# Kernel optimization log

Measured on AMD Instinct MI355X. Metric: run time of the kernel, lower is better.

## Reference

```python
import jax, jax.numpy as jnp
import numpy as np

N = 50000
NEG_SLOPE = 0.2
BN_EPS = 1e-5


def _self_loops(src, dst, n):
    loop = jnp.arange(n, dtype=src.dtype)
    return jnp.concatenate([src, loop]), jnp.concatenate([dst, loop])


def gcn_conv(x, src, dst, W, b, n):
    # PyG GCNConv: add self-loops, symmetric deg^-1/2 normalization, scatter-add.
    h = x @ W                                             # [N, C]
    s, d = _self_loops(src, dst, n)
    deg = jax.ops.segment_sum(jnp.ones_like(d, dtype=h.dtype), d, num_segments=n)
    dinv = jnp.where(deg > 0, jax.lax.rsqrt(deg), 0.0)
    norm = dinv[s] * dinv[d]                              # [E+N]
    out = jax.ops.segment_sum(h[s] * norm[:, None], d, num_segments=n)
    return out + b


def gat_conv(x, src, dst, W, a_src, a_dst, b, n, heads):
    # PyG GATConv (concat=False, eval mode: no dropout): add self-loops,
    # per-edge LeakyReLU attention logits, segment-softmax over dst, mean heads.
    C = W.shape[1] // heads
    h = (x @ W).reshape(n, heads, C)                      # [N, H, C]
    s, d = _self_loops(src, dst, n)
    al_s = jnp.sum(h * a_src[None], axis=-1)              # [N, H]
    al_d = jnp.sum(h * a_dst[None], axis=-1)              # [N, H]
    e = jax.nn.leaky_relu(al_s[s] + al_d[d], NEG_SLOPE)   # [E+N, H]
    emax = jax.ops.segment_max(e, d, num_segments=n)[d]
    ex = jnp.exp(e - emax)
    denom = jax.ops.segment_sum(ex, d, num_segments=n)[d]
    alpha = ex / denom                                    # [E+N, H]
    out = jax.ops.segment_sum(h[s] * alpha[:, :, None], d, num_segments=n)
    return jnp.mean(out, axis=1) + b                      # concat=False -> head mean


def batch_norm(x, g, b, m, v):
    # eval-mode BatchNorm1d with running stats
    return (x - m) * jax.lax.rsqrt(v + BN_EPS) * g + b


def setup_inputs() -> dict:
    key = jax.random.key(0)
    ks = jax.random.split(key, 12)
    E = 800000
    inp = {}
    inp['x'] = jax.random.normal(ks[0], (N, 128), dtype=jnp.float32)
    inp['edge_index'] = jax.random.randint(ks[1], (2, E), 0, N, dtype=jnp.int64)
    inp['gcn1_W'] = jax.random.normal(ks[2], (128, 96), dtype=jnp.float32) * 0.08
    inp['gcn1_b'] = jnp.zeros((96,), jnp.float32)
    inp['bn1_g'] = jnp.ones((96,), jnp.float32)
    inp['bn1_b'] = jnp.zeros((96,), jnp.float32)
    inp['bn1_m'] = jnp.zeros((96,), jnp.float32)
    inp['bn1_v'] = jnp.ones((96,), jnp.float32)
    inp['gat1_W'] = jax.random.normal(ks[3], (96, 192), dtype=jnp.float32) * 0.1
    inp['gat1_as'] = jax.random.normal(ks[4], (2, 96), dtype=jnp.float32) * 0.1
    inp['gat1_ad'] = jax.random.normal(ks[5], (2, 96), dtype=jnp.float32) * 0.1
    inp['gat1_b'] = jnp.zeros((96,), jnp.float32)
    inp['gcn2_W'] = jax.random.normal(ks[6], (96, 96), dtype=jnp.float32) * 0.1
    inp['gcn2_b'] = jnp.zeros((96,), jnp.float32)
    inp['bn2_g'] = jnp.ones((96,), jnp.float32)
    inp['bn2_b'] = jnp.zeros((96,), jnp.float32)
    inp['bn2_m'] = jnp.zeros((96,), jnp.float32)
    inp['bn2_v'] = jnp.ones((96,), jnp.float32)
    inp['gat2_W'] = jax.random.normal(ks[7], (96, 80), dtype=jnp.float32) * 0.1
    inp['gat2_as'] = jax.random.normal(ks[8], (2, 40), dtype=jnp.float32) * 0.1
    inp['gat2_ad'] = jax.random.normal(ks[9], (2, 40), dtype=jnp.float32) * 0.1
    inp['gat2_b'] = jnp.zeros((40,), jnp.float32)
    return inp


def reference(x, edge_index, gcn1_W, gcn1_b, bn1_g, bn1_b, bn1_m, bn1_v,
              gat1_W, gat1_as, gat1_ad, gat1_b, gcn2_W, gcn2_b,
              bn2_g, bn2_b, bn2_m, bn2_v, gat2_W, gat2_as, gat2_ad, gat2_b):
    src, dst = edge_index[0], edge_index[1]
    h = gcn_conv(x, src, dst, gcn1_W, gcn1_b, N)
    h = jax.nn.relu(batch_norm(h, bn1_g, bn1_b, bn1_m, bn1_v))
    h = jax.nn.relu(gat_conv(h, src, dst, gat1_W, gat1_as, gat1_ad, gat1_b, N, 2))
    h = gcn_conv(h, src, dst, gcn2_W, gcn2_b, N)
    h = jax.nn.relu(batch_norm(h, bn2_g, bn2_b, bn2_m, bn2_v))
    h = gat_conv(h, src, dst, gat2_W, gat2_as, gat2_ad, gat2_b, N, 2)
    return jax.nn.log_softmax(h, axis=1)
```

## Files before the change

### kernel.cpp

```cpp
#include <hip/hip_runtime.h>
#include <math.h>

#define NNODES 50000
#define NEG_SLOPE 0.2f
#define BN_EPS 1e-5f

typedef __attribute__((ext_vector_type(8))) short bf16x8;
typedef __attribute__((ext_vector_type(4))) float f32x4;

static __device__ __forceinline__ float leaky(float x) {
    return x > 0.f ? x : NEG_SLOPE * x;
}
static __device__ __forceinline__ unsigned short f2bf(float x) {
    unsigned u = __float_as_uint(x);
    u += 0x7FFFu + ((u >> 16) & 1u);
    return (unsigned short)(u >> 16);
}
static __device__ __forceinline__ void unpack8(uint4 u, float* v) {
    v[0] = __uint_as_float(u.x << 16);
    v[1] = __uint_as_float(u.x & 0xFFFF0000u);
    v[2] = __uint_as_float(u.y << 16);
    v[3] = __uint_as_float(u.y & 0xFFFF0000u);
    v[4] = __uint_as_float(u.z << 16);
    v[5] = __uint_as_float(u.z & 0xFFFF0000u);
    v[6] = __uint_as_float(u.w << 16);
    v[7] = __uint_as_float(u.w & 0xFFFF0000u);
}
static __device__ __forceinline__ void acc8(uint4 u, float w, float* a) {
    float v[8]; unpack8(u, v);
#pragma unroll
    for (int j = 0; j < 8; ++j) a[j] = fmaf(w, v[j], a[j]);
}
static __device__ __forceinline__ uint4 pack8(const float* o) {
    uint4 r;
    r.x = ((unsigned)f2bf(o[1]) << 16) | f2bf(o[0]);
    r.y = ((unsigned)f2bf(o[3]) << 16) | f2bf(o[2]);
    r.z = ((unsigned)f2bf(o[5]) << 16) | f2bf(o[4]);
    r.w = ((unsigned)f2bf(o[7]) << 16) | f2bf(o[6]);
    return r;
}

__global__ void k_count(const int* __restrict__ dst, int* degi, int E) {
    int e = blockIdx.x * blockDim.x + threadIdx.x;
    if (e < E) atomicAdd(&degi[dst[e]], 1);
}
__global__ void k_scan1(const int* __restrict__ degi, int* __restrict__ incl,
                        int* __restrict__ bsum, int n) {
    __shared__ int s[256];
    int i = blockIdx.x * 256 + threadIdx.x;
    int v = (i < n) ? degi[i] : 0;
    s[threadIdx.x] = v;
    __syncthreads();
    for (int off = 1; off < 256; off <<= 1) {
        int t = (threadIdx.x >= (unsigned)off) ? s[threadIdx.x - off] : 0;
        __syncthreads();
        s[threadIdx.x] += t;
        __syncthreads();
    }
    if (i < n) incl[i] = s[threadIdx.x];
    if (threadIdx.x == 255) bsum[blockIdx.x] = s[255];
}
__global__ void k_scan2(int* bsum, int nb) {
    __shared__ int s[256];
    int v = ((int)threadIdx.x < nb) ? bsum[threadIdx.x] : 0;
    s[threadIdx.x] = v;
    __syncthreads();
    for (int off = 1; off < 256; off <<= 1) {
        int t = (threadIdx.x >= (unsigned)off) ? s[threadIdx.x - off] : 0;
        __syncthreads();
        s[threadIdx.x] += t;
        __syncthreads();
    }
    if ((int)threadIdx.x < nb) bsum[threadIdx.x] = s[threadIdx.x];
}
__global__ void k_scan3(const int* __restrict__ degi, const int* __restrict__ incl,
                        const int* __restrict__ bsum, int* __restrict__ row_ptr,
                        int* __restrict__ cursor, float* __restrict__ dinv, int n) {
    int i = blockIdx.x * 256 + threadIdx.x;
    if (i >= n) return;
    int off = (blockIdx.x > 0) ? bsum[blockIdx.x - 1] : 0;
    int inc = incl[i] + off;
    row_ptr[i + 1] = inc;
    cursor[i] = inc - degi[i];
    dinv[i] = rsqrtf((float)(degi[i] + 1));
    if (i == 0) row_ptr[0] = 0;
}
__global__ void k_fill(const int* __restrict__ src, const int* __restrict__ dst,
                       int* cursor, int* __restrict__ csr_src, int E) {
    int e = blockIdx.x * blockDim.x + threadIdx.x;
    if (e >= E) return;
    int pos = atomicAdd(&cursor[dst[e]], 1);
    csr_src[pos] = src[e];
}

__global__ void k_wconv(const float* __restrict__ W, unsigned short* __restrict__ out,
                        int Ki, int Ko) {
    int idx = blockIdx.x * blockDim.x + threadIdx.x;
    if (idx >= Ki * Ko) return;
    int k = idx / Ko, c = idx % Ko;
    out[c * Ki + k] = f2bf(W[idx]);
}
__global__ void k_xconv(const float4* __restrict__ x, uint4* __restrict__ out, int n8) {
    int i = blockIdx.x * blockDim.x + threadIdx.x;
    if (i >= n8) return;
    float4 a = x[i * 2], b = x[i * 2 + 1];
    float o[8] = {a.x, a.y, a.z, a.w, b.x, b.y, b.z, b.w};
    out[i] = pack8(o);
}

template<int KI, int KO>
__launch_bounds__(256)
__global__ void k_gemm_mfma(const unsigned short* __restrict__ A,
                            const unsigned short* __restrict__ WT,
                            unsigned short* __restrict__ C, int n) {
    constexpr int KP = KI + 8;
    constexpr int NT = KO / 16;
    constexpr int KT = KI / 32;
    __shared__ unsigned short wT[KO][KP];
    const int t = threadIdx.x;
    const int w = t >> 6, l = t & 63;

    constexpr int CH = KI / 8;
    for (int idx = t; idx < KO * CH; idx += 256) {
        int r = idx / CH, o = idx % CH;
        *(uint4*)&wT[r][o * 8] = *(const uint4*)&WT[r * KI + o * 8];
    }
    int row = blockIdx.x * 64 + w * 16 + (l & 15);
    bool rv = row < n;
    const unsigned short* ap = A + (long long)row * KI + (l >> 4) * 8;
    bf16x8 afr[KT];
#pragma unroll
    for (int kt = 0; kt < KT; ++kt) {
        bf16x8 z = {};
        afr[kt] = rv ? *(const bf16x8*)(ap + kt * 32) : z;
    }
    __syncthreads();

    f32x4 acc[NT];
#pragma unroll
    for (int ct = 0; ct < NT; ++ct) acc[ct] = (f32x4){0.f, 0.f, 0.f, 0.f};
#pragma unroll
    for (int kt = 0; kt < KT; ++kt) {
#pragma unroll
        for (int ct = 0; ct < NT; ++ct) {
            bf16x8 b = *(const bf16x8*)&wT[ct * 16 + (l & 15)][kt * 32 + (l >> 4) * 8];
            acc[ct] = __builtin_amdgcn_mfma_f32_16x16x32_bf16(afr[kt], b, acc[ct], 0, 0, 0);
        }
    }
    int orow0 = blockIdx.x * 64 + w * 16 + (l >> 4) * 4;
    int col = l & 15;
#pragma unroll
    for (int ct = 0; ct < NT; ++ct) {
#pragma unroll
        for (int r = 0; r < 4; ++r) {
            int rr = orow0 + r;
            if (rr < n) C[(long long)rr * KO + ct * 16 + col] = f2bf(acc[ct][r]);
        }
    }
}

__global__ void k_gcn_gather_bn8(const uint4* __restrict__ hb, const int* __restrict__ row_ptr,
                                 const int* __restrict__ csr_src, const float* __restrict__ dinv,
                                 const float* __restrict__ bias, const float* __restrict__ g,
                                 const float* __restrict__ b, const float* __restrict__ m,
                                 const float* __restrict__ vv,
                                 uint4* __restrict__ outb, int n, int Q8) {
    int t = blockIdx.x * blockDim.x + threadIdx.x;
    if (t >= n * Q8) return;
    int v = t / Q8, q = t % Q8;
    int beg = row_ptr[v], end = row_ptr[v + 1];
    float dv = dinv[v];
    float a[8] = {0.f, 0.f, 0.f, 0.f, 0.f, 0.f, 0.f, 0.f};
    acc8(hb[(long long)v * Q8 + q], dv, a);
    int p = beg;
    for (; p + 4 <= end; p += 4) {
        int s0 = csr_src[p], s1 = csr_src[p + 1], s2 = csr_src[p + 2], s3 = csr_src[p + 3];
        float w0 = dinv[s0], w1 = dinv[s1], w2 = dinv[s2], w3 = dinv[s3];
        uint4 u0 = hb[(long long)s0 * Q8 + q];
        uint4 u1 = hb[(long long)s1 * Q8 + q];
        uint4 u2 = hb[(long long)s2 * Q8 + q];
        uint4 u3 = hb[(long long)s3 * Q8 + q];
        acc8(u0, w0, a);
        acc8(u1, w1, a);
        acc8(u2, w2, a);
        acc8(u3, w3, a);
    }
    for (; p < end; ++p) {
        int s = csr_src[p];
        acc8(hb[(long long)s * Q8 + q], dinv[s], a);
    }
    int c0 = q * 8;
    float o[8];
#pragma unroll
    for (int j = 0; j < 8; ++j) {
        int c = c0 + j;
        float x = fmaf(a[j], dv, bias[c]);
        x = (x - m[c]) * rsqrtf(vv[c] + BN_EPS) * g[c] + b[c];
        o[j] = fmaxf(x, 0.f);
    }
    outb[(long long)v * Q8 + q] = pack8(o);
}

__global__ void k_gat_logits8(const uint4* __restrict__ hb, const float* __restrict__ as,
                              const float* __restrict__ ad, float* __restrict__ alS,
                              float* __restrict__ alD, int n, int C) {
    int t = blockIdx.x * blockDim.x + threadIdx.x;
    if (t >= n * 2) return;
    int hh = t & 1;
    int C8 = C >> 3;
    const uint4* row = hb + (long long)t * C8;
    float s1 = 0.f, s2 = 0.f;
    for (int q = 0; q < C8; ++q) {
        float v[8]; unpack8(row[q], v);
#pragma unroll
        for (int j = 0; j < 8; ++j) {
            int c = hh * C + q * 8 + j;
            s1 = fmaf(v[j], as[c], s1);
            s2 = fmaf(v[j], ad[c], s2);
        }
    }
    alS[t] = s1; alD[t] = s2;
}
__global__ void k_gat_vh2p(const int* __restrict__ row_ptr, const int* __restrict__ csr_src,
                           const float2* __restrict__ alS2, const float2* __restrict__ alD2,
                           float2* __restrict__ eex2, float2* __restrict__ selfw2,
                           float2* __restrict__ invden2, int n) {
    int v = blockIdx.x * blockDim.x + threadIdx.x;
    if (v >= n) return;
    int beg = row_ptr[v], end = row_ptr[v + 1];
    float2 ad = alD2[v], as0 = alS2[v];
    float ls0 = leaky(as0.x + ad.x), ls1 = leaky(as0.y + ad.y);
    float m0 = ls0, m1 = ls1;
    int p = beg;
    for (; p + 2 <= end; p += 2) {
        int s0 = csr_src[p], s1 = csr_src[p + 1];
        float2 a0 = alS2[s0], a1 = alS2[s1];
        float l00 = leaky(a0.x + ad.x), l01 = leaky(a0.y + ad.y);
        float l10 = leaky(a1.x + ad.x), l11 = leaky(a1.y + ad.y);
        eex2[p] = make_float2(l00, l01);
        eex2[p + 1] = make_float2(l10, l11);
        m0 = fmaxf(m0, fmaxf(l00, l10));
        m1 = fmaxf(m1, fmaxf(l01, l11));
    }
    if (p < end) {
        int s = csr_src[p];
        float2 a = alS2[s];
        float l0 = leaky(a.x + ad.x), l1 = leaky(a.y + ad.y);
        eex2[p] = make_float2(l0, l1);
        m0 = fmaxf(m0, l0);
        m1 = fmaxf(m1, l1);
    }
    float e0 = expf(ls0 - m0), e1 = expf(ls1 - m1);
    float d0 = e0, d1 = e1;
    for (p = beg; p < end; ++p) {
        float2 l = eex2[p];
        float x0 = expf(l.x - m0), x1 = expf(l.y - m1);
        eex2[p] = make_float2(x0, x1);
        d0 += x0; d1 += x1;
    }
    selfw2[v] = make_float2(e0, e1);
    invden2[v] = make_float2(1.f / d0, 1.f / d1);
}
template<int OUTBF>
__global__ void k_gat_gather2_8(const uint4* __restrict__ hb, const int* __restrict__ row_ptr,
                                const int* __restrict__ csr_src, const float2* __restrict__ eex2,
                                const float2* __restrict__ selfw2, const float2* __restrict__ invden2,
                                const float* __restrict__ bias, uint4* __restrict__ outb,
                                float4* __restrict__ outf, int n, int Q8, int do_relu) {
    int t = blockIdx.x * blockDim.x + threadIdx.x;
    if (t >= n * Q8) return;
    int v = t / Q8, q = t % Q8;
    int rowOct = 2 * Q8;
    int beg = row_ptr[v], end = row_ptr[v + 1];
    float A0[8] = {0,0,0,0,0,0,0,0}, A1[8] = {0,0,0,0,0,0,0,0};
    {
        float2 sw = selfw2[v];
        const uint4* hv = hb + (long long)v * rowOct;
        acc8(hv[q], sw.x, A0);
        acc8(hv[Q8 + q], sw.y, A1);
    }
    int p = beg;
    for (; p + 4 <= end; p += 4) {
        int s0 = csr_src[p], s1 = csr_src[p + 1], s2 = csr_src[p + 2], s3 = csr_src[p + 3];
        float2 w0 = eex2[p], w1 = eex2[p + 1], w2 = eex2[p + 2], w3 = eex2[p + 3];
        const uint4* h0 = hb + (long long)s0 * rowOct;
        const uint4* h1 = hb + (long long)s1 * rowOct;
        const uint4* h2 = hb + (long long)s2 * rowOct;
        const uint4* h3 = hb + (long long)s3 * rowOct;
        uint4 u00 = h0[q], u01 = h0[Q8 + q];
        uint4 u10 = h1[q], u11 = h1[Q8 + q];
        uint4 u20 = h2[q], u21 = h2[Q8 + q];
        uint4 u30 = h3[q], u31 = h3[Q8 + q];
        acc8(u00, w0.x, A0); acc8(u01, w0.y, A1);
        acc8(u10, w1.x, A0); acc8(u11, w1.y, A1);
        acc8(u20, w2.x, A0); acc8(u21, w2.y, A1);
        acc8(u30, w3.x, A0); acc8(u31, w3.y, A1);
    }
    for (; p < end; ++p) {
        int s = csr_src[p];
        float2 w = eex2[p];
        const uint4* hs = hb + (long long)s * rowOct;
        acc8(hs[q], w.x, A0);
        acc8(hs[Q8 + q], w.y, A1);
    }
    float2 idn = invden2[v];
    int c0 = q * 8;
    float o[8];
#pragma unroll
    for (int j = 0; j < 8; ++j) {
        float x = fmaf(0.5f, fmaf(A0[j], idn.x, A1[j] * idn.y), bias[c0 + j]);
        o[j] = do_relu ? fmaxf(x, 0.f) : x;
    }
    if (OUTBF) {
        outb[(long long)v * Q8 + q] = pack8(o);
    } else {
        long long ob = (long long)v * (Q8 * 2) + q * 2;
        outf[ob]     = make_float4(o[0], o[1], o[2], o[3]);
        outf[ob + 1] = make_float4(o[4], o[5], o[6], o[7]);
    }
}

__global__ void k_logsoftmax40(const float* __restrict__ in, float* __restrict__ out, int n) {
    int v = blockIdx.x * blockDim.x + threadIdx.x;
    if (v >= n) return;
    float vals[40];
    float mx = -INFINITY;
#pragma unroll
    for (int c = 0; c < 40; ++c) {
        float x = in[v * 40 + c];
        vals[c] = x;
        mx = fmaxf(mx, x);
    }
    float s = 0.f;
#pragma unroll
    for (int c = 0; c < 40; ++c) s += expf(vals[c] - mx);
    float ls = logf(s);
#pragma unroll
    for (int c = 0; c < 40; ++c) out[v * 40 + c] = vals[c] - mx - ls;
}

static inline int nblk(long long n, int b) { return (int)((n + b - 1) / b); }

extern "C" void kernel_launch(void* const* d_in, const int* in_sizes, int n_in,
                              void* d_out, int out_size, void* d_ws, size_t ws_size,
                              hipStream_t stream) {
    const float* x       = (const float*)d_in[0];
    const int*   ei      = (const int*)d_in[1];
    const float* gcn1_W  = (const float*)d_in[2];
    const float* gcn1_b  = (const float*)d_in[3];
    const float* bn1_g   = (const float*)d_in[4];
    const float* bn1_b   = (const float*)d_in[5];
    const float* bn1_m   = (const float*)d_in[6];
    const float* bn1_v   = (const float*)d_in[7];
    const float* gat1_W  = (const float*)d_in[8];
    const float* gat1_as = (const float*)d_in[9];
    const float* gat1_ad = (const float*)d_in[10];
    const float* gat1_b  = (const float*)d_in[11];
    const float* gcn2_W  = (const float*)d_in[12];
    const float* gcn2_b  = (const float*)d_in[13];
    const float* bn2_g   = (const float*)d_in[14];
    const float* bn2_b   = (const float*)d_in[15];
    const float* bn2_m   = (const float*)d_in[16];
    const float* bn2_v   = (const float*)d_in[17];
    const float* gat2_W  = (const float*)d_in[18];
    const float* gat2_as = (const float*)d_in[19];
    const float* gat2_ad = (const float*)d_in[20];
    const float* gat2_b  = (const float*)d_in[21];

    const int n = NNODES;
    const int E = in_sizes[1] / 2;
    const int* src = ei;
    const int* dst = ei + E;

    char* p = (char*)d_ws;
    float* dinv    = (float*)p; p += 50048 * 4;
    int*   degi    = (int*)p;   p += 50048 * 4;
    int*   row_ptr = (int*)p;   p += 50052 * 4;
    int*   cursor  = (int*)p;   p += 50048 * 4;
    int*   incl    = (int*)p;   p += 50048 * 4;
    int*   bsum    = (int*)p;   p += 256 * 4;
    int*   csr_src = (int*)p;   p += 800000 * 4;
    unsigned short* hbf = (unsigned short*)p; p += 9600000 * 2;
    unsigned short* abf = (unsigned short*)p; p += 6400000 * 2;
    unsigned short* wbf = (unsigned short*)p; p += 47616 * 2 + 64;
    float* bufA    = (float*)p; p += 2000000 * 4;
    float* alS     = (float*)p; p += 100096 * 4;
    float* alD     = (float*)p; p += 100096 * 4;
    float* selfw   = (float*)p; p += 100096 * 4;
    float* invden  = (float*)p; p += 100096 * 4;
    float* eex     = (float*)p; p += 1600000 * 4;

    unsigned short* w1T = wbf;
    unsigned short* w2T = wbf + 12288;
    unsigned short* w3T = wbf + 12288 + 18432;
    unsigned short* w4T = wbf + 12288 + 18432 + 9216;

    const int B = 256;
    const int GB = nblk(n, 64);
    const int SB = nblk(n, 256);
    float* out = (float*)d_out;

    k_wconv<<<nblk(128 * 96, B), B, 0, stream>>>(gcn1_W, w1T, 128, 96);
    k_wconv<<<nblk(96 * 192, B), B, 0, stream>>>(gat1_W, w2T, 96, 192);
    k_wconv<<<nblk(96 * 96, B), B, 0, stream>>>(gcn2_W, w3T, 96, 96);
    k_wconv<<<nblk(96 * 80, B), B, 0, stream>>>(gat2_W, w4T, 96, 80);
    k_xconv<<<nblk((long long)n * 16, B), B, 0, stream>>>((const float4*)x, (uint4*)abf, n * 16);

    hipMemsetAsync(degi, 0, (size_t)n * 4, stream);
    k_count<<<nblk(E, B), B, 0, stream>>>(dst, degi, E);
    k_scan1<<<SB, 256, 0, stream>>>(degi, incl, bsum, n);
    k_scan2<<<1, 256, 0, stream>>>(bsum, SB);
    k_scan3<<<SB, 256, 0, stream>>>(degi, incl, bsum, row_ptr, cursor, dinv, n);
    k_fill<<<nblk(E, B), B, 0, stream>>>(src, dst, cursor, csr_src, E);

    k_gemm_mfma<128, 96><<<GB, 256, 0, stream>>>(abf, w1T, hbf, n);
    k_gcn_gather_bn8<<<nblk((long long)n * 12, B), B, 0, stream>>>(
        (const uint4*)hbf, row_ptr, csr_src, dinv, gcn1_b, bn1_g, bn1_b, bn1_m, bn1_v,
        (uint4*)abf, n, 12);

    k_gemm_mfma<96, 192><<<GB, 256, 0, stream>>>(abf, w2T, hbf, n);
    k_gat_logits8<<<nblk(n * 2, B), B, 0, stream>>>((const uint4*)hbf, gat1_as, gat1_ad, alS, alD, n, 96);
    k_gat_vh2p<<<nblk(n, B), B, 0, stream>>>(row_ptr, csr_src, (const float2*)alS, (const float2*)alD,
                                             (float2*)eex, (float2*)selfw, (float2*)invden, n);
    k_gat_gather2_8<1><<<nblk((long long)n * 12, B), B, 0, stream>>>(
        (const uint4*)hbf, row_ptr, csr_src, (const float2*)eex, (const float2*)selfw,
        (const float2*)invden, gat1_b, (uint4*)abf, nullptr, n, 12, 1);

    k_gemm_mfma<96, 96><<<GB, 256, 0, stream>>>(abf, w3T, hbf, n);
    k_gcn_gather_bn8<<<nblk((long long)n * 12, B), B, 0, stream>>>(
        (const uint4*)hbf, row_ptr, csr_src, dinv, gcn2_b, bn2_g, bn2_b, bn2_m, bn2_v,
        (uint4*)abf, n, 12);

    k_gemm_mfma<96, 80><<<GB, 256, 0, stream>>>(abf, w4T, hbf, n);
    k_gat_logits8<<<nblk(n * 2, B), B, 0, stream>>>((const uint4*)hbf, gat2_as, gat2_ad, alS, alD, n, 40);
    k_gat_vh2p<<<nblk(n, B), B, 0, stream>>>(row_ptr, csr_src, (const float2*)alS, (const float2*)alD,
                                             (float2*)eex, (float2*)selfw, (float2*)invden, n);
    k_gat_gather2_8<0><<<nblk((long long)n * 5, B), B, 0, stream>>>(
        (const uint4*)hbf, row_ptr, csr_src, (const float2*)eex, (const float2*)selfw,
        (const float2*)invden, gat2_b, nullptr, (float4*)bufA, n, 5, 0);

    k_logsoftmax40<<<nblk(n, B), B, 0, stream>>>(bufA, out, n);
}
```

Baseline: 375.4 us.

## Fuse GAT logits into GEMM epilogue, merge conversions, use nontemporal loads/stores

Computes GAT attention logits inside the MFMA GEMM epilogue from fp32 accumulators using cross-lane shuffles, removing the separate logits kernel and its reread of the bf16 features. Merges the four weight conversions and the x conversion into one launch. Switches streaming CSR/edge-weight loads and output stores to nontemporal hints to reduce cache pollution. Logits now come from fp32 rather than bf16-rounded values, which changes numerics slightly; nontemporal stores of outputs reread by the next GEMM may lose cache reuse.

```diff
diff --git a/kernel.cpp b/kernel.cpp
--- a/kernel.cpp
+++ b/kernel.cpp
@@ -7,6 +7,7 @@
 
 typedef __attribute__((ext_vector_type(8))) short bf16x8;
 typedef __attribute__((ext_vector_type(4))) float f32x4;
+typedef __attribute__((ext_vector_type(4))) unsigned int u32x4;
 
 static __device__ __forceinline__ float leaky(float x) {
     return x > 0.f ? x : NEG_SLOPE * x;
@@ -38,6 +39,19 @@
     r.z = ((unsigned)f2bf(o[5]) << 16) | f2bf(o[4]);
     r.w = ((unsigned)f2bf(o[7]) << 16) | f2bf(o[6]);
     return r;
+}
+static __device__ __forceinline__ int ldnt_i(const int* p) {
+    return __builtin_nontemporal_load(p);
+}
+static __device__ __forceinline__ float2 ldnt_f2(const float2* p) {
+    unsigned long long d = __builtin_nontemporal_load((const unsigned long long*)p);
+    return make_float2(__uint_as_float((unsigned)d), __uint_as_float((unsigned)(d >> 32)));
+}
+static __device__ __forceinline__ void stnt_u4(uint4* p, uint4 v) {
+    __builtin_nontemporal_store(*(u32x4*)&v, (u32x4*)p);
+}
+static __device__ __forceinline__ void stnt_f4(float4* p, float4 v) {
+    __builtin_nontemporal_store(*(f32x4*)&v, (f32x4*)p);
 }
 
 __global__ void k_count(const int* __restrict__ dst, int* degi, int E) {
@@ -93,26 +107,42 @@
     csr_src[pos] = src[e];
 }
 
-__global__ void k_wconv(const float* __restrict__ W, unsigned short* __restrict__ out,
-                        int Ki, int Ko) {
-    int idx = blockIdx.x * blockDim.x + threadIdx.x;
-    if (idx >= Ki * Ko) return;
-    int k = idx / Ko, c = idx % Ko;
-    out[c * Ki + k] = f2bf(W[idx]);
-}
-__global__ void k_xconv(const float4* __restrict__ x, uint4* __restrict__ out, int n8) {
+__global__ void k_convall(const float4* __restrict__ x, uint4* __restrict__ xout,
+                          const float* __restrict__ W1, unsigned short* __restrict__ w1T,
+                          const float* __restrict__ W2, unsigned short* __restrict__ w2T,
+                          const float* __restrict__ W3, unsigned short* __restrict__ w3T,
+                          const float* __restrict__ W4, unsigned short* __restrict__ w4T,
+                          int nx) {
     int i = blockIdx.x * blockDim.x + threadIdx.x;
-    if (i >= n8) return;
-    float4 a = x[i * 2], b = x[i * 2 + 1];
-    float o[8] = {a.x, a.y, a.z, a.w, b.x, b.y, b.z, b.w};
-    out[i] = pack8(o);
-}
-
-template<int KI, int KO>
+    if (i < nx) {
+        float4 a = x[i * 2], b = x[i * 2 + 1];
+        float o[8] = {a.x, a.y, a.z, a.w, b.x, b.y, b.z, b.w};
+        xout[i] = pack8(o);
+        return;
+    }
+    int j = i - nx;
+    if (j < 12288) {
+        int k = j / 96, c = j % 96;
+        w1T[c * 128 + k] = f2bf(W1[j]);
+    } else if ((j -= 12288) < 18432) {
+        int k = j / 192, c = j % 192;
+        w2T[c * 96 + k] = f2bf(W2[j]);
+    } else if ((j -= 18432) < 9216) {
+        int k = j / 96, c = j % 96;
+        w3T[c * 96 + k] = f2bf(W3[j]);
+    } else if ((j -= 9216) < 7680) {
+        int k = j / 80, c = j % 80;
+        w4T[c * 96 + k] = f2bf(W4[j]);
+    }
+}
+
+template<int KI, int KO, int HC>
 __launch_bounds__(256)
 __global__ void k_gemm_mfma(const unsigned short* __restrict__ A,
                             const unsigned short* __restrict__ WT,
-                            unsigned short* __restrict__ C, int n) {
+                            unsigned short* __restrict__ C, int n,
+                            const float* __restrict__ as, const float* __restrict__ ad,
+                            float* __restrict__ alS, float* __restrict__ alD) {
     constexpr int KP = KI + 8;
     constexpr int NT = KO / 16;
     constexpr int KT = KI / 32;
@@ -155,6 +185,38 @@
         for (int r = 0; r < 4; ++r) {
             int rr = orow0 + r;
             if (rr < n) C[(long long)rr * KO + ct * 16 + col] = f2bf(acc[ct][r]);
+        }
+    }
+    if (HC > 0) {
+        float asv[NT], adv[NT];
+#pragma unroll
+        for (int ct = 0; ct < NT; ++ct) {
+            int cg = ct * 16 + col;
+            asv[ct] = as[cg];
+            adv[ct] = ad[cg];
+        }
+#pragma unroll
+        for (int r = 0; r < 4; ++r) {
+            float s0 = 0.f, s1 = 0.f, d0 = 0.f, d1 = 0.f;
+#pragma unroll
+            for (int ct = 0; ct < NT; ++ct) {
+                int cg = ct * 16 + col;
+                float v = acc[ct][r];
+                if (cg < HC) { s0 = fmaf(v, asv[ct], s0); d0 = fmaf(v, adv[ct], d0); }
+                else         { s1 = fmaf(v, asv[ct], s1); d1 = fmaf(v, adv[ct], d1); }
+            }
+#pragma unroll
+            for (int m = 1; m < 16; m <<= 1) {
+                s0 += __shfl_xor(s0, m);
+                s1 += __shfl_xor(s1, m);
+                d0 += __shfl_xor(d0, m);
+                d1 += __shfl_xor(d1, m);
+            }
+            int rr = orow0 + r;
+            if ((l & 15) == 0 && rr < n) {
+                alS[rr * 2] = s0; alS[rr * 2 + 1] = s1;
+                alD[rr * 2] = d0; alD[rr * 2 + 1] = d1;
+            }
         }
     }
 }
@@ -174,7 +236,8 @@
     acc8(hb[(long long)v * Q8 + q], dv, a);
     int p = beg;
     for (; p + 4 <= end; p += 4) {
-        int s0 = csr_src[p], s1 = csr_src[p + 1], s2 = csr_src[p + 2], s3 = csr_src[p + 3];
+        int s0 = ldnt_i(&csr_src[p]),     s1 = ldnt_i(&csr_src[p + 1]);
+        int s2 = ldnt_i(&csr_src[p + 2]), s3 = ldnt_i(&csr_src[p + 3]);
         float w0 = dinv[s0], w1 = dinv[s1], w2 = dinv[s2], w3 = dinv[s3];
         uint4 u0 = hb[(long long)s0 * Q8 + q];
         uint4 u1 = hb[(long long)s1 * Q8 + q];
@@ -186,7 +249,7 @@
         acc8(u3, w3, a);
     }
     for (; p < end; ++p) {
-        int s = csr_src[p];
+        int s = ldnt_i(&csr_src[p]);
         acc8(hb[(long long)s * Q8 + q], dinv[s], a);
     }
     int c0 = q * 8;
@@ -198,29 +261,9 @@
         x = (x - m[c]) * rsqrtf(vv[c] + BN_EPS) * g[c] + b[c];
         o[j] = fmaxf(x, 0.f);
     }
-    outb[(long long)v * Q8 + q] = pack8(o);
-}
-
-__global__ void k_gat_logits8(const uint4* __restrict__ hb, const float* __restrict__ as,
-                              const float* __restrict__ ad, float* __restrict__ alS,
-                              float* __restrict__ alD, int n, int C) {
-    int t = blockIdx.x * blockDim.x + threadIdx.x;
-    if (t >= n * 2) return;
-    int hh = t & 1;
-    int C8 = C >> 3;
-    const uint4* row = hb + (long long)t * C8;
-    float s1 = 0.f, s2 = 0.f;
-    for (int q = 0; q < C8; ++q) {
-        float v[8]; unpack8(row[q], v);
-#pragma unroll
-        for (int j = 0; j < 8; ++j) {
-            int c = hh * C + q * 8 + j;
-            s1 = fmaf(v[j], as[c], s1);
-            s2 = fmaf(v[j], ad[c], s2);
-        }
-    }
-    alS[t] = s1; alD[t] = s2;
-}
+    stnt_u4(&outb[(long long)v * Q8 + q], pack8(o));
+}
+
 __global__ void k_gat_vh2p(const int* __restrict__ row_ptr, const int* __restrict__ csr_src,
                            const float2* __restrict__ alS2, const float2* __restrict__ alD2,
                            float2* __restrict__ eex2, float2* __restrict__ selfw2,
@@ -281,8 +324,10 @@
     }
     int p = beg;
     for (; p + 4 <= end; p += 4) {
-        int s0 = csr_src[p], s1 = csr_src[p + 1], s2 = csr_src[p + 2], s3 = csr_src[p + 3];
-        float2 w0 = eex2[p], w1 = eex2[p + 1], w2 = eex2[p + 2], w3 = eex2[p + 3];
+        int s0 = ldnt_i(&csr_src[p]),     s1 = ldnt_i(&csr_src[p + 1]);
+        int s2 = ldnt_i(&csr_src[p + 2]), s3 = ldnt_i(&csr_src[p + 3]);
+        float2 w0 = ldnt_f2(&eex2[p]),     w1 = ldnt_f2(&eex2[p + 1]);
+        float2 w2 = ldnt_f2(&eex2[p + 2]), w3 = ldnt_f2(&eex2[p + 3]);
         const uint4* h0 = hb + (long long)s0 * rowOct;
         const uint4* h1 = hb + (long long)s1 * rowOct;
         const uint4* h2 = hb + (long long)s2 * rowOct;
@@ -297,8 +342,8 @@
         acc8(u30, w3.x, A0); acc8(u31, w3.y, A1);
     }
     for (; p < end; ++p) {
-        int s = csr_src[p];
-        float2 w = eex2[p];
+        int s = ldnt_i(&csr_src[p]);
+        float2 w = ldnt_f2(&eex2[p]);
         const uint4* hs = hb + (long long)s * rowOct;
         acc8(hs[q], w.x, A0);
         acc8(hs[Q8 + q], w.y, A1);
@@ -312,11 +357,11 @@
         o[j] = do_relu ? fmaxf(x, 0.f) : x;
     }
     if (OUTBF) {
-        outb[(long long)v * Q8 + q] = pack8(o);
+        stnt_u4(&outb[(long long)v * Q8 + q], pack8(o));
     } else {
         long long ob = (long long)v * (Q8 * 2) + q * 2;
-        outf[ob]     = make_float4(o[0], o[1], o[2], o[3]);
-        outf[ob + 1] = make_float4(o[4], o[5], o[6], o[7]);
+        stnt_f4(&outf[ob],     make_float4(o[0], o[1], o[2], o[3]));
+        stnt_f4(&outf[ob + 1], make_float4(o[4], o[5], o[6], o[7]));
     }
 }
 
@@ -400,11 +445,9 @@
     const int SB = nblk(n, 256);
     float* out = (float*)d_out;
 
-    k_wconv<<<nblk(128 * 96, B), B, 0, stream>>>(gcn1_W, w1T, 128, 96);
-    k_wconv<<<nblk(96 * 192, B), B, 0, stream>>>(gat1_W, w2T, 96, 192);
-    k_wconv<<<nblk(96 * 96, B), B, 0, stream>>>(gcn2_W, w3T, 96, 96);
-    k_wconv<<<nblk(96 * 80, B), B, 0, stream>>>(gat2_W, w4T, 96, 80);
-    k_xconv<<<nblk((long long)n * 16, B), B, 0, stream>>>((const float4*)x, (uint4*)abf, n * 16);
+    const int NX = n * 16;
+    k_convall<<<nblk(NX + 47616, B), B, 0, stream>>>(
+        (const float4*)x, (uint4*)abf, gcn1_W, w1T, gat1_W, w2T, gcn2_W, w3T, gat2_W, w4T, NX);
 
     hipMemsetAsync(degi, 0, (size_t)n * 4, stream);
     k_count<<<nblk(E, B), B, 0, stream>>>(dst, degi, E);
@@ -413,26 +456,24 @@
     k_scan3<<<SB, 256, 0, stream>>>(degi, incl, bsum, row_ptr, cursor, dinv, n);
     k_fill<<<nblk(E, B), B, 0, stream>>>(src, dst, cursor, csr_src, E);
 
-    k_gemm_mfma<128, 96><<<GB, 256, 0, stream>>>(abf, w1T, hbf, n);
+    k_gemm_mfma<128, 96, 0><<<GB, 256, 0, stream>>>(abf, w1T, hbf, n, nullptr, nullptr, nullptr, nullptr);
     k_gcn_gather_bn8<<<nblk((long long)n * 12, B), B, 0, stream>>>(
         (const uint4*)hbf, row_ptr, csr_src, dinv, gcn1_b, bn1_g, bn1_b, bn1_m, bn1_v,
         (uint4*)abf, n, 12);
 
-    k_gemm_mfma<96, 192><<<GB, 256, 0, stream>>>(abf, w2T, hbf, n);
-    k_gat_logits8<<<nblk(n * 2, B), B, 0, stream>>>((const uint4*)hbf, gat1_as, gat1_ad, alS, alD, n, 96);
+    k_gemm_mfma<96, 192, 96><<<GB, 256, 0, stream>>>(abf, w2T, hbf, n, gat1_as, gat1_ad, alS, alD);
     k_gat_vh2p<<<nblk(n, B), B, 0, stream>>>(row_ptr, csr_src, (const float2*)alS, (const float2*)alD,
                                              (float2*)eex, (float2*)selfw, (float2*)invden, n);
     k_gat_gather2_8<1><<<nblk((long long)n * 12, B), B, 0, stream>>>(
         (const uint4*)hbf, row_ptr, csr_src, (const float2*)eex, (const float2*)selfw,
         (const float2*)invden, gat1_b, (uint4*)abf, nullptr, n, 12, 1);
 
-    k_gemm_mfma<96, 96><<<GB, 256, 0, stream>>>(abf, w3T, hbf, n);
+    k_gemm_mfma<96, 96, 0><<<GB, 256, 0, stream>>>(abf, w3T, hbf, n, nullptr, nullptr, nullptr, nullptr);
     k_gcn_gather_bn8<<<nblk((long long)n * 12, B), B, 0, stream>>>(
         (const uint4*)hbf, row_ptr, csr_src, dinv, gcn2_b, bn2_g, bn2_b, bn2_m, bn2_v,
         (uint4*)abf, n, 12);
 
-    k_gemm_mfma<96, 80><<<GB, 256, 0, stream>>>(abf, w4T, hbf, n);
-    k_gat_logits8<<<nblk(n * 2, B), B, 0, stream>>>((const uint4*)hbf, gat2_as, gat2_ad, alS, alD, n, 40);
+    k_gemm_mfma<96, 80, 40><<<GB, 256, 0, stream>>>(abf, w4T, hbf, n, gat2_as, gat2_ad, alS, alD);
     k_gat_vh2p<<<nblk(n, B), B, 0, stream>>>(row_ptr, csr_src, (const float2*)alS, (const float2*)alD,
                                              (float2*)eex, (float2*)selfw, (float2*)invden, n);
     k_gat_gather2_8<0><<<nblk((long long)n * 5, B), B, 0, stream>>>(
```

After: 381.8 us. No clear change (+1.7%).
